# Kernel tuning notes

Hardware: AMD Instinct MI355X
Metric: run time of the kernel (lower is better)

## Reference

```python
import jax, jax.numpy as jnp
import numpy as np

FEATURE_HEIGHT = 50
FEATURE_WIDTH = 50


def setup_inputs() -> dict:
    key = jax.random.key(0)
    k1, k2, k3 = jax.random.split(key, 3)
    bs, K, H, D = 16, FEATURE_HEIGHT * FEATURE_WIDTH, 8, 32
    Q, L, P = 2000, 1, 4
    value = jax.random.normal(k1, (bs, K, H, D), dtype=jnp.float32)
    value_spatial_shapes = jnp.array([[FEATURE_HEIGHT, FEATURE_WIDTH]], dtype=jnp.int64)
    sampling_locations = jax.random.uniform(k2, (bs, Q, H, L, P, 2), dtype=jnp.float32)
    attention_weights = jax.random.uniform(k3, (bs, Q, H, L, P), dtype=jnp.float32)
    return {
        "value": value,
        "value_spatial_shapes": value_spatial_shapes,
        "sampling_locations": sampling_locations,
        "attention_weights": attention_weights,
    }


def _bilinear_sample(img, grid):
    """torch.F.grid_sample(mode='bilinear', padding_mode='zeros', align_corners=False).

    img:  (N, D, h, w)
    grid: (N, Q, P, 2), last dim (x, y) in [-1, 1]
    returns (N, D, Q, P)
    """
    N, D, h, w = img.shape
    # unnormalize (align_corners=False)
    x = (grid[..., 0] + 1.0) * (w * 0.5) - 0.5  # (N, Q, P)
    y = (grid[..., 1] + 1.0) * (h * 0.5) - 0.5
    x0 = jnp.floor(x)
    y0 = jnp.floor(y)
    x1 = x0 + 1.0
    y1 = y0 + 1.0
    wx1 = x - x0
    wx0 = 1.0 - wx1
    wy1 = y - y0
    wy0 = 1.0 - wy1

    img_flat = img.reshape(N, D, h * w)

    def corner(ix, iy, wgt):
        valid = ((ix >= 0) & (ix < w) & (iy >= 0) & (iy < h)).astype(img.dtype)
        ixc = jnp.clip(ix, 0, w - 1).astype(jnp.int32)
        iyc = jnp.clip(iy, 0, h - 1).astype(jnp.int32)
        idx = (iyc * w + ixc).reshape(N, -1)  # (N, Q*P)
        vals = jnp.take_along_axis(img_flat, idx[:, None, :], axis=2)  # (N, D, Q*P)
        vals = vals.reshape(N, D, *ix.shape[1:])  # (N, D, Q, P)
        return vals * (wgt * valid)[:, None]

    out = corner(x0, y0, wx0 * wy0)
    out = out + corner(x1, y0, wx1 * wy0)
    out = out + corner(x0, y1, wx0 * wy1)
    out = out + corner(x1, y1, wx1 * wy1)
    return out


def reference(value, value_spatial_shapes, sampling_locations, attention_weights):
    bs, K, H, D = value.shape
    _, Q, _, L, P, _ = sampling_locations.shape
    h, w = FEATURE_HEIGHT, FEATURE_WIDTH

    sampling_grids = 2.0 * sampling_locations - 1.0  # (bs, Q, H, L, P, 2)
    # value -> (bs*H, D, h, w)
    v = value.reshape(bs, K, H * D).transpose(0, 2, 1).reshape(bs * H, D, h, w)
    # level 0 grid -> (bs*H, Q, P, 2)
    g = jnp.transpose(sampling_grids[:, :, :, 0], (0, 2, 1, 3, 4)).reshape(bs * H, Q, P, 2)
    sampled = _bilinear_sample(v, g)  # (bs*H, D, Q, P)
    # attention weights -> (bs*H, 1, Q, L*P)
    aw = jnp.transpose(attention_weights, (0, 2, 1, 3, 4)).reshape(bs * H, 1, Q, L * P)
    out = (sampled * aw).sum(-1)  # (bs*H, D, Q)
    out = out.reshape(bs, H * D, Q).transpose(0, 2, 1)  # (bs, Q, H*D)
    return out
```

## Files before the change

kernel.cpp:

```cpp
#include <hip/hip_runtime.h>


#define FH 50
#define FW 50
#define KK (FH * FW)
#define NH 8
#define ND 32
#define NQ 2000
#define NP 4

#define QPB 8
#define BLOCKS_PER_B (NQ / QPB)

__global__ __launch_bounds__(256, 2) void deform_attn_kernel(
    const float* __restrict__ value,
    const float* __restrict__ loc,
    const float* __restrict__ attw,
    float* __restrict__ out)
{
    const int x = blockIdx.x;
    const int xcd = x & 7;
    const int slot = x >> 3;
    const int phase = (slot >= BLOCKS_PER_B) ? 1 : 0;
    const int b = xcd + (phase << 3);
    const int q0 = (slot - phase * BLOCKS_PER_B) * QPB;

    const int t = threadIdx.x;
    const int c = t & 7;
    const int lg = t >> 3;
    const int h = lg & 7;
    const int qo = lg >> 3;

    const char* __restrict__ vb =
        (const char*)(value + (size_t)b * KK * NH * ND);
    const int hc = h * (ND * 4) + c * 16;

    const int qA = q0 + qo;
    const int gidA = (b * NQ + qA) * NH + h;

    float4 accA = {0.f, 0.f, 0.f, 0.f};
    float4 accB = {0.f, 0.f, 0.f, 0.f};

    auto sample = [&](int gid, float4& acc) {
        const float4* __restrict__ lp = (const float4*)loc + (size_t)gid * 2;
        const float4 l0 = lp[0];
        const float4 l1 = lp[1];
        const float4 a4 = ((const float4*)attw)[gid];

        const float pxx[NP] = {l0.x, l0.z, l1.x, l1.z};
        const float pyy[NP] = {l0.y, l0.w, l1.y, l1.w};
        const float awp[NP] = {a4.x, a4.y, a4.z, a4.w};

        unsigned offs[16];
        float wts[16];
#pragma unroll
        for (int p = 0; p < NP; ++p) {
            const float fx = pxx[p] * (float)FW - 0.5f;
            const float fy = pyy[p] * (float)FH - 0.5f;
            const float x0f = floorf(fx);
            const float y0f = floorf(fy);
            const int x0 = (int)x0f, y0 = (int)y0f;
            const int x1 = x0 + 1, y1 = y0 + 1;
            const float wx1 = fx - x0f, wx0 = 1.f - wx1;
            const float wy1 = fy - y0f, wy0 = 1.f - wy1;

            const bool vx0 = (x0 >= 0) & (x0 < FW);
            const bool vx1 = (x1 >= 0) & (x1 < FW);
            const bool vy0 = (y0 >= 0) & (y0 < FH);
            const bool vy1 = (y1 >= 0) & (y1 < FH);

            const int cx0 = min(max(x0, 0), FW - 1);
            const int cx1 = min(max(x1, 0), FW - 1);
            const int cy0 = min(max(y0, 0), FH - 1);
            const int cy1 = min(max(y1, 0), FH - 1);

            offs[p * 4 + 0] = (unsigned)((cy0 * FW + cx0) * 1024 + hc);
            offs[p * 4 + 1] = (unsigned)((cy0 * FW + cx1) * 1024 + hc);
            offs[p * 4 + 2] = (unsigned)((cy1 * FW + cx0) * 1024 + hc);
            offs[p * 4 + 3] = (unsigned)((cy1 * FW + cx1) * 1024 + hc);

            wts[p * 4 + 0] = ((vx0 & vy0) ? (wx0 * wy0) : 0.f) * awp[p];
            wts[p * 4 + 1] = ((vx1 & vy0) ? (wx1 * wy0) : 0.f) * awp[p];
            wts[p * 4 + 2] = ((vx0 & vy1) ? (wx0 * wy1) : 0.f) * awp[p];
            wts[p * 4 + 3] = ((vx1 & vy1) ? (wx1 * wy1) : 0.f) * awp[p];
        }

        float4 v[16];
#pragma unroll
        for (int i = 0; i < 16; ++i)
            v[i] = *(const float4*)(vb + offs[i]);
#pragma unroll
        for (int i = 0; i < 16; ++i) {
            acc.x += wts[i] * v[i].x;
            acc.y += wts[i] * v[i].y;
            acc.z += wts[i] * v[i].z;
            acc.w += wts[i] * v[i].w;
        }
    };

    sample(gidA, accA);
    sample(gidA + 4 * NH, accB);

    float4* __restrict__ op = (float4*)out;
    op[(size_t)(b * NQ + qA) * (NH * ND / 4) + h * (ND / 4) + c] = accA;
    op[(size_t)(b * NQ + qA + 4) * (NH * ND / 4) + h * (ND / 4) + c] = accB;
}

extern "C" void kernel_launch(void* const* d_in, const int* in_sizes, int n_in,
                              void* d_out, int out_size, void* d_ws, size_t ws_size,
                              hipStream_t stream) {
    const float* value = (const float*)d_in[0];
    const float* loc  = (const float*)d_in[2];
    const float* attw = (const float*)d_in[3];
    float* out = (float*)d_out;

    const int blocks = 16 * BLOCKS_PER_B;
    deform_attn_kernel<<<blocks, 256, 0, stream>>>(value, loc, attw, out);
}
```

Baseline: 120.4 us.

## Issue all 32 gathers up front with inline asm and staged vmcnt waits

Loads all location and weight vectors for both queries first, then issues the 16 value gathers for query A and the 16 for query B back-to-back using inline global_load_dwordx4 with an SGPR base. Manual s_waitcnt vmcnt(16) and vmcnt(0) with sched barriers let the accumulation for A overlap the in-flight loads for B. The aim is more memory-level parallelism per thread. The cost is higher register pressure (32 float4 in flight) under launch_bounds(256,2), which could cause spills or lower occupancy. Inline asm also makes correctness depend on the manual wait counts, since the compiler cannot track these loads.

```diff
diff --git a/kernel.cpp b/kernel.cpp
--- a/kernel.cpp
+++ b/kernel.cpp
@@ -11,6 +11,8 @@
 
 #define QPB 8
 #define BLOCKS_PER_B (NQ / QPB)
+
+typedef float f32x4 __attribute__((ext_vector_type(4)));
 
 __global__ __launch_bounds__(256, 2) void deform_attn_kernel(
     const float* __restrict__ value,
@@ -31,28 +33,27 @@
     const int h = lg & 7;
     const int qo = lg >> 3;
 
-    const char* __restrict__ vb =
-        (const char*)(value + (size_t)b * KK * NH * ND);
+    const float* __restrict__ vbase = value + (size_t)b * (KK * NH * ND);
     const int hc = h * (ND * 4) + c * 16;
 
     const int qA = q0 + qo;
     const int gidA = (b * NQ + qA) * NH + h;
+    const int gidB = gidA + 4 * NH;
 
-    float4 accA = {0.f, 0.f, 0.f, 0.f};
-    float4 accB = {0.f, 0.f, 0.f, 0.f};
+    f32x4 l0A = ((const f32x4*)loc)[(size_t)gidA * 2 + 0];
+    f32x4 l1A = ((const f32x4*)loc)[(size_t)gidA * 2 + 1];
+    f32x4 l0B = ((const f32x4*)loc)[(size_t)gidB * 2 + 0];
+    f32x4 l1B = ((const f32x4*)loc)[(size_t)gidB * 2 + 1];
+    f32x4 aA = ((const f32x4*)attw)[gidA];
+    f32x4 aB = ((const f32x4*)attw)[gidB];
+    asm volatile("" : "+v"(l0A), "+v"(l1A), "+v"(aA),
+                      "+v"(l0B), "+v"(l1B), "+v"(aB));
 
-    auto sample = [&](int gid, float4& acc) {
-        const float4* __restrict__ lp = (const float4*)loc + (size_t)gid * 2;
-        const float4 l0 = lp[0];
-        const float4 l1 = lp[1];
-        const float4 a4 = ((const float4*)attw)[gid];
-
+    auto computeOW = [&](const f32x4 l0, const f32x4 l1, const f32x4 a4,
+                         unsigned* offs, float* wts) {
         const float pxx[NP] = {l0.x, l0.z, l1.x, l1.z};
         const float pyy[NP] = {l0.y, l0.w, l1.y, l1.w};
         const float awp[NP] = {a4.x, a4.y, a4.z, a4.w};
-
-        unsigned offs[16];
-        float wts[16];
 #pragma unroll
         for (int p = 0; p < NP; ++p) {
             const float fx = pxx[p] * (float)FW - 0.5f;
@@ -84,24 +85,44 @@
             wts[p * 4 + 2] = ((vx0 & vy1) ? (wx0 * wy1) : 0.f) * awp[p];
             wts[p * 4 + 3] = ((vx1 & vy1) ? (wx1 * wy1) : 0.f) * awp[p];
         }
-
-        float4 v[16];
-#pragma unroll
-        for (int i = 0; i < 16; ++i)
-            v[i] = *(const float4*)(vb + offs[i]);
-#pragma unroll
-        for (int i = 0; i < 16; ++i) {
-            acc.x += wts[i] * v[i].x;
-            acc.y += wts[i] * v[i].y;
-            acc.z += wts[i] * v[i].z;
-            acc.w += wts[i] * v[i].w;
-        }
     };
 
-    sample(gidA, accA);
-    sample(gidA + 4 * NH, accB);
+    unsigned offsA[16]; float wtsA[16];
+    computeOW(l0A, l1A, aA, offsA, wtsA);
 
-    float4* __restrict__ op = (float4*)out;
+    f32x4 vA[16];
+#pragma unroll
+    for (int i = 0; i < 16; ++i)
+        asm volatile("global_load_dwordx4 %0, %1, %2"
+                     : "=v"(vA[i]) : "v"(offsA[i]), "s"(vbase));
+
+    unsigned offsB[16]; float wtsB[16];
+    computeOW(l0B, l1B, aB, offsB, wtsB);
+
+    f32x4 vB[16];
+#pragma unroll
+    for (int i = 0; i < 16; ++i)
+        asm volatile("global_load_dwordx4 %0, %1, %2"
+                     : "=v"(vB[i]) : "v"(offsB[i]), "s"(vbase));
+
+    f32x4 accA = {0.f, 0.f, 0.f, 0.f};
+    f32x4 accB = {0.f, 0.f, 0.f, 0.f};
+
+    __builtin_amdgcn_sched_barrier(0);
+    asm volatile("s_waitcnt vmcnt(16)" ::: "memory");
+    __builtin_amdgcn_sched_barrier(0);
+#pragma unroll
+    for (int i = 0; i < 16; ++i)
+        accA += vA[i] * wtsA[i];
+
+    __builtin_amdgcn_sched_barrier(0);
+    asm volatile("s_waitcnt vmcnt(0)" ::: "memory");
+    __builtin_amdgcn_sched_barrier(0);
+#pragma unroll
+    for (int i = 0; i < 16; ++i)
+        accB += vB[i] * wtsB[i];
+
+    f32x4* __restrict__ op = (f32x4*)out;
     op[(size_t)(b * NQ + qA) * (NH * ND / 4) + h * (ND / 4) + c] = accA;
     op[(size_t)(b * NQ + qA + 4) * (NH * ND / 4) + h * (ND / 4) + c] = accB;
 }
```

After: 117.8 us. 1.02x faster.

## Stage per-head value channel slice in LDS and gather bilinear corners from shared memory

Applied to the files above, without the earlier changes.

The grid is remapped so each block owns one (batch, head, 4-channel group) and first copies that head's 2500 float4 value slice into 40KB of LDS. Each thread then loops over queries and performs its 16 bilinear corner gathers from LDS instead of from global memory. The goal is to swap latency-bound random global/L2 gathers for LDS reads. In exchange, sampling locations and attention weights are re-read once per channel group, giving 8x redundant traffic. Per-thread loads and output stores are also strided rather than coalesced, and LDS size limits occupancy to about 4 blocks per CU.

```diff
diff --git a/kernel.cpp b/kernel.cpp
--- a/kernel.cpp
+++ b/kernel.cpp
@@ -8,50 +8,56 @@
 #define ND 32
 #define NQ 2000
 #define NP 4
+#define TPB 256
+#define NPASS ((NQ + TPB - 1) / TPB)
 
-#define QPB 8
-#define BLOCKS_PER_B (NQ / QPB)
+typedef float f32x4 __attribute__((ext_vector_type(4)));
 
-__global__ __launch_bounds__(256, 2) void deform_attn_kernel(
+__global__ __launch_bounds__(TPB, 4) void deform_attn_kernel(
     const float* __restrict__ value,
     const float* __restrict__ loc,
     const float* __restrict__ attw,
     float* __restrict__ out)
 {
-    const int x = blockIdx.x;
-    const int xcd = x & 7;
-    const int slot = x >> 3;
-    const int phase = (slot >= BLOCKS_PER_B) ? 1 : 0;
-    const int b = xcd + (phase << 3);
-    const int q0 = (slot - phase * BLOCKS_PER_B) * QPB;
+    const int id = blockIdx.x;
+    const int cg = id >> 7;
+    const int bh = id & 127;
+    const int b  = bh >> 3;
+    const int h  = bh & 7;
+
+    __shared__ f32x4 lds[KK];
 
     const int t = threadIdx.x;
-    const int c = t & 7;
-    const int lg = t >> 3;
-    const int h = lg & 7;
-    const int qo = lg >> 3;
 
-    const char* __restrict__ vb =
-        (const char*)(value + (size_t)b * KK * NH * ND);
-    const int hc = h * (ND * 4) + c * 16;
+    {
+        const f32x4* __restrict__ src =
+            (const f32x4*)value + (size_t)b * KK * 64 + h * 8 + cg;
+#pragma unroll
+        for (int i = 0; i < 10; ++i) {
+            const int k = i * TPB + t;
+            if (k < KK) lds[k] = src[(size_t)k * 64];
+        }
+    }
+    __syncthreads();
 
-    const int qA = q0 + qo;
-    const int gidA = (b * NQ + qA) * NH + h;
+    const f32x4* __restrict__ lp = (const f32x4*)loc;
+    const f32x4* __restrict__ ap = (const f32x4*)attw;
+    f32x4* __restrict__ op = (f32x4*)out;
 
-    float4 accA = {0.f, 0.f, 0.f, 0.f};
-    float4 accB = {0.f, 0.f, 0.f, 0.f};
+    for (int pass = 0; pass < NPASS; ++pass) {
+        const int q = pass * TPB + t;
+        if (q >= NQ) break;
 
-    auto sample = [&](int gid, float4& acc) {
-        const float4* __restrict__ lp = (const float4*)loc + (size_t)gid * 2;
-        const float4 l0 = lp[0];
-        const float4 l1 = lp[1];
-        const float4 a4 = ((const float4*)attw)[gid];
+        const int gid = (b * NQ + q) * NH + h;
+        const f32x4 l0 = lp[(size_t)gid * 2 + 0];
+        const f32x4 l1 = lp[(size_t)gid * 2 + 1];
+        const f32x4 a4 = ap[gid];
 
         const float pxx[NP] = {l0.x, l0.z, l1.x, l1.z};
         const float pyy[NP] = {l0.y, l0.w, l1.y, l1.w};
         const float awp[NP] = {a4.x, a4.y, a4.z, a4.w};
 
-        unsigned offs[16];
+        int   idx[16];
         float wts[16];
 #pragma unroll
         for (int p = 0; p < NP; ++p) {
@@ -74,10 +80,10 @@
             const int cy0 = min(max(y0, 0), FH - 1);
             const int cy1 = min(max(y1, 0), FH - 1);
 
-            offs[p * 4 + 0] = (unsigned)((cy0 * FW + cx0) * 1024 + hc);
-            offs[p * 4 + 1] = (unsigned)((cy0 * FW + cx1) * 1024 + hc);
-            offs[p * 4 + 2] = (unsigned)((cy1 * FW + cx0) * 1024 + hc);
-            offs[p * 4 + 3] = (unsigned)((cy1 * FW + cx1) * 1024 + hc);
+            idx[p * 4 + 0] = cy0 * FW + cx0;
+            idx[p * 4 + 1] = cy0 * FW + cx1;
+            idx[p * 4 + 2] = cy1 * FW + cx0;
+            idx[p * 4 + 3] = cy1 * FW + cx1;
 
             wts[p * 4 + 0] = ((vx0 & vy0) ? (wx0 * wy0) : 0.f) * awp[p];
             wts[p * 4 + 1] = ((vx1 & vy0) ? (wx1 * wy0) : 0.f) * awp[p];
@@ -85,25 +91,18 @@
             wts[p * 4 + 3] = ((vx1 & vy1) ? (wx1 * wy1) : 0.f) * awp[p];
         }
 
-        float4 v[16];
-#pragma unroll
-        for (int i = 0; i < 16; ++i)
-            v[i] = *(const float4*)(vb + offs[i]);
+        f32x4 acc = {0.f, 0.f, 0.f, 0.f};
 #pragma unroll
         for (int i = 0; i < 16; ++i) {
-            acc.x += wts[i] * v[i].x;
-            acc.y += wts[i] * v[i].y;
-            acc.z += wts[i] * v[i].z;
-            acc.w += wts[i] * v[i].w;
+            const f32x4 v = lds[idx[i]];
+            acc.x += wts[i] * v.x;
+            acc.y += wts[i] * v.y;
+            acc.z += wts[i] * v.z;
+            acc.w += wts[i] * v.w;
         }
-    };
 
-    sample(gidA, accA);
-    sample(gidA + 4 * NH, accB);
-
-    float4* __restrict__ op = (float4*)out;
-    op[(size_t)(b * NQ + qA) * (NH * ND / 4) + h * (ND / 4) + c] = accA;
-    op[(size_t)(b * NQ + qA + 4) * (NH * ND / 4) + h * (ND / 4) + c] = accB;
+        op[(size_t)(b * NQ + q) * 64 + h * 8 + cg] = acc;
+    }
 }
 
 extern "C" void kernel_launch(void* const* d_in, const int* in_sizes, int n_in,
@@ -114,6 +113,6 @@
     const float* attw = (const float*)d_in[3];
     float* out = (float*)d_out;
 
-    const int blocks = 16 * BLOCKS_PER_B;
-    deform_attn_kernel<<<blocks, 256, 0, stream>>>(value, loc, attw, out);
+    const int blocks = 8 * 16 * 8;
+    deform_attn_kernel<<<blocks, TPB, 0, stream>>>(value, loc, attw, out);
 }
```

Result: slower. 154.6 us (+28.5%).
